# Performance work log

Measured on AMD Instinct MI355X. Metric: run time of the kernel, lower is better.

## Reference

```python
import jax, jax.numpy as jnp
import numpy as np

N = 100_000      # nodes
E = 500_000      # bonds
DN = 128         # dim_node_embedding
DB = 64          # dim_bond_embedding
NTOK = 4         # num_bond_token
DIN = 2 * DN + 2 * DB  # 384
LEAKY = 0.001
LN_EPS = 1e-5
DIST_MAX = 20.0
STEP = 0.5


def _lrelu(v):
    return jnp.where(v >= 0, v, LEAKY * v)


def _layernorm(v, w, b):
    m = v.mean(-1, keepdims=True)
    var = ((v - m) ** 2).mean(-1, keepdims=True)
    return (v - m) / jnp.sqrt(var + LN_EPS) * w + b


def setup_inputs() -> dict:
    key = jax.random.key(0)
    ks = jax.random.split(key, 20)
    x = jax.random.normal(ks[0], (N, 3), dtype=jnp.float32) * 3.0
    pos = jax.random.normal(ks[1], (N, 3), dtype=jnp.float32)
    node_embedding = jax.random.normal(ks[2], (N, DN), dtype=jnp.float32)
    i0 = jax.random.randint(ks[3], (E,), 0, N)
    off = jax.random.randint(ks[4], (E,), 1, N)  # nonzero -> no self-bonds
    bond_index = jnp.stack([i0, (i0 + off) % N], axis=1).astype(jnp.int32)
    bond_types = jax.random.randint(ks[5], (E,), 0, NTOK).astype(jnp.int32)
    s = 0.02
    params = dict(
        bond_emb=jax.random.normal(ks[6], (NTOK, DB), dtype=jnp.float32),
        W0=jax.random.normal(ks[7], (DIN, DN), dtype=jnp.float32) * s,
        b0=jnp.zeros((DN,), jnp.float32),
        W1=jax.random.normal(ks[8], (DN, DN), dtype=jnp.float32) * s,
        b1=jnp.zeros((DN,), jnp.float32),
        ln1_w=jnp.ones((DN,), jnp.float32),
        ln1_b=jnp.zeros((DN,), jnp.float32),
        W2=jax.random.normal(ks[9], (DN, DN), dtype=jnp.float32) * s,
        b2=jnp.zeros((DN,), jnp.float32),
        ln2_w=jnp.ones((DN,), jnp.float32),
        ln2_b=jnp.zeros((DN,), jnp.float32),
        Wo=jax.random.normal(ks[10], (DN, 2), dtype=jnp.float32) * s,
        bo=jnp.zeros((2,), jnp.float32),
    )
    return dict(x=x, pos=pos, node_embedding=node_embedding,
                bond_index=bond_index, bond_types=bond_types, **params)


def reference(x, pos, node_embedding, bond_index, bond_types,
              bond_emb, W0, b0, W1, b1, ln1_w, ln1_b,
              W2, b2, ln2_w, ln2_b, Wo, bo):
    i = bond_index[:, 0]
    j = bond_index[:, 1]

    # ---- BondLength geometry ----
    diff = x[i] - x[j]                                   # [E,3]
    dist = jnp.linalg.norm(diff, axis=-1, keepdims=True)  # [E,1]
    u = diff / dist                                       # [E,3] unit j->i? (i-j)/d
    direction = jnp.stack([u, -u], axis=-1)               # [E,3,2]

    # ---- Smearing (gaussian RBF + overflow bin, normalized) ----
    offset = jnp.linspace(0.0, DIST_MAX, DB - 1, dtype=jnp.float32)  # [63]
    delta = DIST_MAX / (DB - 2)
    coeff = -0.5 / (delta * delta)
    rbf = jnp.exp(coeff * (dist - offset) ** 2)            # [E,63]
    ovf = (dist >= DIST_MAX).astype(x.dtype)               # [E,1]
    smear = jnp.concatenate([rbf, ovf], axis=-1)           # [E,64]
    smear = smear / smear.sum(axis=-1, keepdims=True)

    # ---- Edge MLP (LeakyMLP, num_layer=2, dim_end=2) ----
    feat = jnp.concatenate(
        [node_embedding[i], node_embedding[j], bond_emb[bond_types], smear],
        axis=-1)                                           # [E,384]
    h = _lrelu(feat @ W0 + b0)
    h = _lrelu(_layernorm(h @ W1 + b1, ln1_w, ln1_b))
    h = _lrelu(_layernorm(h @ W2 + b2, ln2_w, ln2_b))
    force = h @ Wo + bo                                    # [E,2]

    # ---- position update (scatter-add) ----
    update = force[:, None, :] * direction                 # [E,3,2]
    pos = pos.at[i].add(STEP * update[..., 0])
    pos = pos.at[j].add(STEP * update[..., 1])
    return pos
```

## Files before the change

### kernel.cpp

```cpp
#include <hip/hip_runtime.h>
#include <stdint.h>

#define N_EDGES 500000
#define N_NODES 100000

typedef __attribute__((ext_vector_type(8))) short short8;
typedef __attribute__((ext_vector_type(4))) float floatx4;

__device__ __forceinline__ uint16_t f2bf(float f) {
  union { float f; uint32_t u; } cv; cv.f = f;
  uint32_t u = cv.u;
  return (uint16_t)((u + 0x7FFFu + ((u >> 16) & 1u)) >> 16);
}
__device__ __forceinline__ uint32_t pk2bf(float lo, float hi) {
  return __builtin_amdgcn_perm(__float_as_uint(hi), __float_as_uint(lo), 0x07060302u);
}
__device__ __forceinline__ uint16_t bftrunc(float f) {
  return (uint16_t)(__float_as_uint(f) >> 16);
}
__device__ __forceinline__ float bf2f_lo(uint32_t u) {
  return __uint_as_float(u << 16);
}
__device__ __forceinline__ float bf2f_hi(uint32_t u) {
  return __uint_as_float(u & 0xFFFF0000u);
}
__device__ __forceinline__ float lrelu(float v) { return fmaxf(v, 0.001f * v); }

__global__ void prep0_kernel(const float* __restrict__ W0, const float* __restrict__ b0,
                             const float* __restrict__ W1, const float* __restrict__ W2,
                             const float* __restrict__ bemb,
                             uint16_t* __restrict__ w0ab, uint16_t* __restrict__ w0c,
                             uint16_t* __restrict__ w1f, uint16_t* __restrict__ w2f,
                             float* __restrict__ be0f,
                             const float* __restrict__ pos, float* __restrict__ out, int npos) {
  int id = blockIdx.x * 256 + threadIdx.x;
  if (id < 32768) {
    int f = id;
    int j = f & 7, lane = (f >> 3) & 63, ntt = (f >> 9) & 15, ks = f >> 13;
    int k = ks * 32 + (lane >> 4) * 8 + j;
    int row = (ntt < 8) ? k : (128 + k);
    int col = (ntt & 7) * 16 + (lane & 15);
    w0ab[f] = f2bf(W0[row * 128 + col]);
  } else if (id < 40960) {
    int f = id - 32768;
    int j = f & 7, lane = (f >> 3) & 63, nt = (f >> 9) & 7, ks = f >> 12;
    int k = ks * 32 + (lane >> 4) * 8 + j;
    w0c[f] = f2bf(W0[(320 + k) * 128 + nt * 16 + (lane & 15)]);
  } else if (id < 57344) {
    int f = id - 40960;
    int j = f & 7, lane = (f >> 3) & 63, nt = (f >> 9) & 7, ks = f >> 12;
    int k = ks * 32 + (lane >> 4) * 8 + j;
    w1f[f] = f2bf(W1[k * 128 + nt * 16 + (lane & 15)]);
  } else if (id < 73728) {
    int f = id - 57344;
    int j = f & 7, lane = (f >> 3) & 63, nt = (f >> 9) & 7, ks = f >> 12;
    int k = ks * 32 + (lane >> 4) * 8 + j;
    w2f[f] = f2bf(W2[k * 128 + nt * 16 + (lane & 15)]);
  } else if (id < 74240) {
    int t = id - 73728; int ty = t >> 7, n = t & 127;
    float s = b0[n];
    for (int kk = 0; kk < 64; ++kk) s += bemb[ty * 64 + kk] * W0[(256 + kk) * 128 + n];
    be0f[t] = s;
  } else if (id - 74240 < npos) {
    out[id - 74240] = pos[id - 74240];
  }
}

__global__ __attribute__((amdgpu_flat_work_group_size(256, 256), amdgpu_waves_per_eu(3, 3)))
void prep_p_kernel(const float* __restrict__ nemb, const uint16_t* __restrict__ w0ab,
                   uint16_t* __restrict__ Pa, uint16_t* __restrict__ Pb) {
  __shared__ __align__(16) uint16_t aLds[4 * 16 * 136];
  const int tid = threadIdx.x;
  const int lane = tid & 63;
  const int wave = tid >> 6;
  const int n15 = lane & 15;
  const int quad = lane >> 4;
  uint16_t* myA = aLds + wave * (16 * 136);
  const int base = blockIdx.x * 64 + wave * 16;

  {
    const int le = lane >> 2, sub = lane & 3;
    int r = base + le; if (r >= N_NODES) r = N_NODES - 1;
    const float4* src = (const float4*)(nemb + (size_t)r * 128);
#pragma unroll
    for (int g = 0; g < 4; ++g) {
      float4 a = src[sub * 8 + g * 2], b = src[sub * 8 + g * 2 + 1];
      uint4 pk;
      pk.x = pk2bf(a.x, a.y); pk.y = pk2bf(a.z, a.w);
      pk.z = pk2bf(b.x, b.y); pk.w = pk2bf(b.z, b.w);
      *(uint4*)(myA + le * 136 + sub * 32 + g * 8) = pk;
    }
  }

  floatx4 acc[16];
#pragma unroll
  for (int t = 0; t < 16; ++t) acc[t] = (floatx4){0.f, 0.f, 0.f, 0.f};
  const short8* wfv = (const short8*)w0ab + lane;
#pragma unroll
  for (int ks = 0; ks < 4; ++ks) {
    short8 a = *(const short8*)(myA + n15 * 136 + ks * 32 + quad * 8);
    short8 b[16];
#pragma unroll
    for (int ntt = 0; ntt < 16; ++ntt) b[ntt] = wfv[(ks * 16 + ntt) * 64];
#pragma unroll
    for (int ntt = 0; ntt < 16; ++ntt)
      acc[ntt] = __builtin_amdgcn_mfma_f32_16x16x32_bf16(a, b[ntt], acc[ntt], 0, 0, 0);
  }

#pragma unroll
  for (int p = 0; p < 2; ++p) {
#pragma unroll
    for (int nt = 0; nt < 8; ++nt)
#pragma unroll
      for (int r = 0; r < 4; ++r)
        myA[(quad * 4 + r) * 136 + nt * 16 + n15] = bftrunc(acc[p * 8 + nt][r]);
    const int le = lane >> 2, sub = lane & 3;
    int row = base + le;
    if (row < N_NODES) {
      uint16_t* dst = (p == 0 ? Pa : Pb) + (size_t)row * 128;
#pragma unroll
      for (int g = 0; g < 4; ++g)
        *(uint4*)(dst + sub * 32 + g * 8) =
            *(const uint4*)(myA + le * 136 + sub * 32 + g * 8);
    }
  }
}

template <int NKS>
__device__ __forceinline__ void gemm_fw(const uint16_t* __restrict__ wf,
                                        const uint16_t* aRow, int lane, floatx4* acc) {
  const short8* wfv = (const short8*)wf + lane;
  short8 a[NKS];
#pragma unroll
  for (int ks = 0; ks < NKS; ++ks) a[ks] = *(const short8*)(aRow + ks * 32);
  short8 b0[8], b1[8];
#pragma unroll
  for (int nt = 0; nt < 8; ++nt) b0[nt] = wfv[nt * 64];
#pragma unroll
  for (int ks = 0; ks < NKS; ++ks) {
    const short8* cur = (ks & 1) ? b1 : b0;
    short8* nxt = (ks & 1) ? b0 : b1;
    if (ks + 1 < NKS) {
#pragma unroll
      for (int nt = 0; nt < 8; ++nt) nxt[nt] = wfv[((ks + 1) * 8 + nt) * 64];
    }
#pragma unroll
    for (int nt = 0; nt < 8; ++nt)
      acc[nt] = __builtin_amdgcn_mfma_f32_16x16x32_bf16(a[ks], cur[nt], acc[nt], 0, 0, 0);
  }
}

__global__ __attribute__((amdgpu_flat_work_group_size(256, 256), amdgpu_waves_per_eu(3, 3)))
void bond_mlp_kernel(const float* __restrict__ x,
                     const int* __restrict__ bidx, const int* __restrict__ btyp,
                     const uint16_t* __restrict__ Pa, const uint16_t* __restrict__ Pb,
                     const uint16_t* __restrict__ w0c, const uint16_t* __restrict__ w1f,
                     const uint16_t* __restrict__ w2f, const float* __restrict__ be0f,
                     const float* __restrict__ b1, const float* __restrict__ ln1w,
                     const float* __restrict__ ln1b,
                     const float* __restrict__ b2, const float* __restrict__ ln2w,
                     const float* __restrict__ ln2b,
                     const float* __restrict__ Wo, const float* __restrict__ bo,
                     float* __restrict__ out) {
  __shared__ __align__(16) uint16_t wlds[4 * 5312];
  __shared__ float u_lds[64][3];
  __shared__ int ij_lds[64][2];
  __shared__ int type_lds[64];

  const int tid = threadIdx.x;
  const int lane = tid & 63;
  const int wave = tid >> 6;
  const int n15 = lane & 15;
  const int quad = lane >> 4;

  uint16_t* base16 = wlds + wave * 5312;
  float* h0pre = (float*)base16;
  uint16_t* hA = base16;
  uint16_t* smearA = base16 + 4160;

  {
    const int le = lane >> 2, sub = lane & 3;
    const int lrow = le;
    const int ge = blockIdx.x * 64 + wave * 16 + le;
    const bool valid = ge < N_EDGES;
    int vi = 0, vj = 0, bt = 0;
    if (valid) { vi = bidx[2 * ge]; vj = bidx[2 * ge + 1]; bt = btyp[ge]; }
    float dx, dy, dz;
    if (valid) {
      dx = x[3 * vi]     - x[3 * vj];
      dy = x[3 * vi + 1] - x[3 * vj + 1];
      dz = x[3 * vi + 2] - x[3 * vj + 2];
    } else { dx = 1.0f; dy = 0.0f; dz = 0.0f; }
    float dist = sqrtf(dx * dx + dy * dy + dz * dz);
    float rinv = 1.0f / dist;
    if (sub == 0) {
      int gr = wave * 16 + lrow;
      u_lds[gr][0] = dx * rinv; u_lds[gr][1] = dy * rinv; u_lds[gr][2] = dz * rinv;
      ij_lds[gr][0] = vi; ij_lds[gr][1] = vj; type_lds[gr] = bt;
    }
    const uint4* pa = (const uint4*)(Pa + (size_t)vi * 128);
    const uint4* pb = (const uint4*)(Pb + (size_t)vj * 128);
    const float4* bbp = (const float4*)(be0f + bt * 128);
#pragma unroll
    for (int g = 0; g < 4; ++g) {
      uint4 av = pa[sub * 4 + g];
      uint4 bv = pb[sub * 4 + g];
      float4 e0 = bbp[sub * 8 + g * 2], e1 = bbp[sub * 8 + g * 2 + 1];
      float4 s0, s1;
      s0.x = bf2f_lo(av.x) + bf2f_lo(bv.x) + e0.x;
      s0.y = bf2f_hi(av.x) + bf2f_hi(bv.x) + e0.y;
      s0.z = bf2f_lo(av.y) + bf2f_lo(bv.y) + e0.z;
      s0.w = bf2f_hi(av.y) + bf2f_hi(bv.y) + e0.w;
      s1.x = bf2f_lo(av.z) + bf2f_lo(bv.z) + e1.x;
      s1.y = bf2f_hi(av.z) + bf2f_hi(bv.z) + e1.y;
      s1.z = bf2f_lo(av.w) + bf2f_lo(bv.w) + e1.z;
      s1.w = bf2f_hi(av.w) + bf2f_hi(bv.w) + e1.w;
      *(float4*)(h0pre + lrow * 130 + sub * 32 + g * 8) = s0;
      *(float4*)(h0pre + lrow * 130 + sub * 32 + g * 8 + 4) = s1;
    }
    const float delta = 20.0f / 62.0f;
    const float coeff = -0.5f / (delta * delta);
    float sv[16]; float ssum = 0.0f;
#pragma unroll
    for (int t = 0; t < 16; ++t) {
      int kk = sub * 16 + t;
      float v;
      if (kk < 63) { float d = dist - (float)kk * delta; v = __expf(coeff * d * d); }
      else v = (dist >= 20.0f) ? 1.0f : 0.0f;
      sv[t] = v; ssum += v;
    }
    ssum += __shfl_xor(ssum, 1);
    ssum += __shfl_xor(ssum, 2);
    float sinv = 1.0f / ssum;
#pragma unroll
    for (int g = 0; g < 2; ++g) {
      uint4 pk;
      pk.x = pk2bf(sv[g*8+0]*sinv, sv[g*8+1]*sinv);
      pk.y = pk2bf(sv[g*8+2]*sinv, sv[g*8+3]*sinv);
      pk.z = pk2bf(sv[g*8+4]*sinv, sv[g*8+5]*sinv);
      pk.w = pk2bf(sv[g*8+6]*sinv, sv[g*8+7]*sinv);
      *(uint4*)(smearA + lrow * 72 + sub * 16 + g * 8) = pk;
    }
  }

  floatx4 acc[8];
#pragma unroll
  for (int nt = 0; nt < 8; ++nt)
#pragma unroll
    for (int r = 0; r < 4; ++r)
      acc[nt][r] = h0pre[(quad * 4 + r) * 130 + nt * 16 + n15];

  gemm_fw<2>(w0c, smearA + n15 * 72 + quad * 8, lane, acc);

#pragma unroll
  for (int nt = 0; nt < 8; ++nt)
#pragma unroll
    for (int r = 0; r < 4; ++r)
      hA[(quad * 4 + r) * 136 + nt * 16 + n15] = bftrunc(lrelu(acc[nt][r]));

#pragma unroll
  for (int nt = 0; nt < 8; ++nt) acc[nt] = (floatx4){0.f, 0.f, 0.f, 0.f};
  gemm_fw<4>(w1f, hA + n15 * 136 + quad * 8, lane, acc);

  {
    float bv[8], wv[8], bb2[8];
#pragma unroll
    for (int nt = 0; nt < 8; ++nt) {
      int col = nt * 16 + n15;
      bv[nt] = b1[col]; wv[nt] = ln1w[col]; bb2[nt] = ln1b[col];
    }
    float s[4] = {0,0,0,0}, q[4] = {0,0,0,0};
#pragma unroll
    for (int nt = 0; nt < 8; ++nt)
#pragma unroll
      for (int r = 0; r < 4; ++r) { float v = acc[nt][r] + bv[nt]; s[r] += v; q[r] += v * v; }
#pragma unroll
    for (int m = 1; m <= 8; m <<= 1)
#pragma unroll
      for (int r = 0; r < 4; ++r) { s[r] += __shfl_xor(s[r], m); q[r] += __shfl_xor(q[r], m); }
    float mean[4], rstd[4];
#pragma unroll
    for (int r = 0; r < 4; ++r) {
      mean[r] = s[r] * (1.0f / 128.0f);
      float var = q[r] * (1.0f / 128.0f) - mean[r] * mean[r];
      rstd[r] = rsqrtf(var + 1e-5f);
    }
#pragma unroll
    for (int nt = 0; nt < 8; ++nt)
#pragma unroll
      for (int r = 0; r < 4; ++r) {
        float v = acc[nt][r] + bv[nt];
        float vn = (v - mean[r]) * rstd[r] * wv[nt] + bb2[nt];
        hA[(quad * 4 + r) * 136 + nt * 16 + n15] = bftrunc(lrelu(vn));
      }
  }

#pragma unroll
  for (int nt = 0; nt < 8; ++nt) acc[nt] = (floatx4){0.f, 0.f, 0.f, 0.f};
  gemm_fw<4>(w2f, hA + n15 * 136 + quad * 8, lane, acc);

  {
    float bv[8], wv[8], bb2[8], wo0[8], wo1[8];
#pragma unroll
    for (int nt = 0; nt < 8; ++nt) {
      int col = nt * 16 + n15;
      bv[nt] = b2[col]; wv[nt] = ln2w[col]; bb2[nt] = ln2b[col];
      wo0[nt] = Wo[2 * col]; wo1[nt] = Wo[2 * col + 1];
    }
    float s[4] = {0,0,0,0}, q[4] = {0,0,0,0};
#pragma unroll
    for (int nt = 0; nt < 8; ++nt)
#pragma unroll
      for (int r = 0; r < 4; ++r) { float v = acc[nt][r] + bv[nt]; s[r] += v; q[r] += v * v; }
#pragma unroll
    for (int m = 1; m <= 8; m <<= 1)
#pragma unroll
      for (int r = 0; r < 4; ++r) { s[r] += __shfl_xor(s[r], m); q[r] += __shfl_xor(q[r], m); }
    float mean[4], rstd[4];
#pragma unroll
    for (int r = 0; r < 4; ++r) {
      mean[r] = s[r] * (1.0f / 128.0f);
      float var = q[r] * (1.0f / 128.0f) - mean[r] * mean[r];
      rstd[r] = rsqrtf(var + 1e-5f);
    }
    float f0[4] = {0,0,0,0}, f1[4] = {0,0,0,0};
#pragma unroll
    for (int nt = 0; nt < 8; ++nt)
#pragma unroll
      for (int r = 0; r < 4; ++r) {
        float v = acc[nt][r] + bv[nt];
        float vn = lrelu((v - mean[r]) * rstd[r] * wv[nt] + bb2[nt]);
        f0[r] += vn * wo0[nt];
        f1[r] += vn * wo1[nt];
      }
#pragma unroll
    for (int m = 1; m <= 8; m <<= 1)
#pragma unroll
      for (int r = 0; r < 4; ++r) { f0[r] += __shfl_xor(f0[r], m); f1[r] += __shfl_xor(f1[r], m); }

    if (n15 < 4) {
      int gr = wave * 16 + quad * 4 + n15;
      int ge2 = blockIdx.x * 64 + gr;
      if (ge2 < N_EDGES) {
        float F0 = (n15 == 0) ? f0[0] : (n15 == 1) ? f0[1] : (n15 == 2) ? f0[2] : f0[3];
        float F1 = (n15 == 0) ? f1[0] : (n15 == 1) ? f1[1] : (n15 == 2) ? f1[2] : f1[3];
        F0 += bo[0]; F1 += bo[1];
        float ux = u_lds[gr][0], uy = u_lds[gr][1], uz = u_lds[gr][2];
        int ii = ij_lds[gr][0], jj = ij_lds[gr][1];
        float c0 = 0.5f * F0;
        float c1 = -0.5f * F1;
        atomicAdd(out + 3 * ii,     c0 * ux);
        atomicAdd(out + 3 * ii + 1, c0 * uy);
        atomicAdd(out + 3 * ii + 2, c0 * uz);
        atomicAdd(out + 3 * jj,     c1 * ux);
        atomicAdd(out + 3 * jj + 1, c1 * uy);
        atomicAdd(out + 3 * jj + 2, c1 * uz);
      }
    }
  }
}

extern "C" void kernel_launch(void* const* d_in, const int* in_sizes, int n_in,
                              void* d_out, int out_size, void* d_ws, size_t ws_size,
                              hipStream_t stream) {
  const float* x    = (const float*)d_in[0];
  const float* pos  = (const float*)d_in[1];
  const float* nemb = (const float*)d_in[2];
  const int*   bidx = (const int*)d_in[3];
  const int*   btyp = (const int*)d_in[4];
  const float* bemb = (const float*)d_in[5];
  const float* W0   = (const float*)d_in[6];
  const float* b0   = (const float*)d_in[7];
  const float* W1   = (const float*)d_in[8];
  const float* b1   = (const float*)d_in[9];
  const float* ln1w = (const float*)d_in[10];
  const float* ln1b = (const float*)d_in[11];
  const float* W2   = (const float*)d_in[12];
  const float* b2   = (const float*)d_in[13];
  const float* ln2w = (const float*)d_in[14];
  const float* ln2b = (const float*)d_in[15];
  const float* Wo   = (const float*)d_in[16];
  const float* bo   = (const float*)d_in[17];
  float* out = (float*)d_out;

  uint16_t* w0ab = (uint16_t*)d_ws;
  uint16_t* w0c  = w0ab + 32768;
  uint16_t* w1f  = w0c + 8192;
  uint16_t* w2f  = w1f + 16384;
  float*    be0f = (float*)(w2f + 16384);
  uint16_t* Pa   = (uint16_t*)(be0f + 512);
  uint16_t* Pb   = Pa + (size_t)N_NODES * 128;

  prep0_kernel<<<(74240 + out_size + 255) / 256, 256, 0, stream>>>(
      W0, b0, W1, W2, bemb, w0ab, w0c, w1f, w2f, be0f, pos, out, out_size);
  prep_p_kernel<<<(N_NODES + 63) / 64, 256, 0, stream>>>(nemb, w0ab, Pa, Pb);
  bond_mlp_kernel<<<(N_EDGES + 63) / 64, 256, 0, stream>>>(
      x, bidx, btyp, Pa, Pb, w0c, w1f, w2f, be0f,
      b1, ln1w, ln1b, b2, ln2w, ln2b, Wo, bo, out);
}
```

Measured before the change: 362.6 us.

## Shrink LDS in bond MLP, batch node rows in prep, drop weight double-buffer

The bond MLP kernel now stores the gathered first-layer partial sums as bf16 instead of fp32 in LDS, which shrinks its per-wave LDS footprint. Its waves_per_eu pin is removed and the weight double-buffer in gemm_fw is dropped to lower register pressure, both aimed at higher occupancy. The node-projection prep kernel processes two 16-row groups per wave, reuses each weight fragment across them, and writes results straight to global memory with scalar 16-bit stores instead of staging through LDS. The bf16 round-trip adds rounding error to the first-layer preactivation, and the scattered 2-byte stores may coalesce poorly.

Result: faster. 353.7 us (-2.4%).

```diff
diff --git a/kernel.cpp b/kernel.cpp
--- a/kernel.cpp
+++ b/kernel.cpp
@@ -3,6 +3,7 @@
 
 #define N_EDGES 500000
 #define N_NODES 100000
+#define PREP_NG 2
 
 typedef __attribute__((ext_vector_type(8))) short short8;
 typedef __attribute__((ext_vector_type(4))) float floatx4;
@@ -17,6 +18,9 @@
 }
 __device__ __forceinline__ uint16_t bftrunc(float f) {
   return (uint16_t)(__float_as_uint(f) >> 16);
+}
+__device__ __forceinline__ float bfup(uint16_t h) {
+  return __uint_as_float(((uint32_t)h) << 16);
 }
 __device__ __forceinline__ float bf2f_lo(uint32_t u) {
   return __uint_as_float(u << 16);
@@ -66,62 +70,67 @@
   }
 }
 
-__global__ __attribute__((amdgpu_flat_work_group_size(256, 256), amdgpu_waves_per_eu(3, 3)))
+__global__ __attribute__((amdgpu_flat_work_group_size(256, 256), amdgpu_waves_per_eu(1, 4)))
 void prep_p_kernel(const float* __restrict__ nemb, const uint16_t* __restrict__ w0ab,
                    uint16_t* __restrict__ Pa, uint16_t* __restrict__ Pb) {
-  __shared__ __align__(16) uint16_t aLds[4 * 16 * 136];
+  __shared__ __align__(16) uint16_t aLds[4 * PREP_NG * 16 * 136];
   const int tid = threadIdx.x;
   const int lane = tid & 63;
   const int wave = tid >> 6;
   const int n15 = lane & 15;
   const int quad = lane >> 4;
-  uint16_t* myA = aLds + wave * (16 * 136);
-  const int base = blockIdx.x * 64 + wave * 16;
+  uint16_t* myA = aLds + wave * (PREP_NG * 16 * 136);
+  const int base = blockIdx.x * (64 * PREP_NG) + wave * (16 * PREP_NG);
 
   {
     const int le = lane >> 2, sub = lane & 3;
-    int r = base + le; if (r >= N_NODES) r = N_NODES - 1;
-    const float4* src = (const float4*)(nemb + (size_t)r * 128);
-#pragma unroll
-    for (int g = 0; g < 4; ++g) {
-      float4 a = src[sub * 8 + g * 2], b = src[sub * 8 + g * 2 + 1];
-      uint4 pk;
-      pk.x = pk2bf(a.x, a.y); pk.y = pk2bf(a.z, a.w);
-      pk.z = pk2bf(b.x, b.y); pk.w = pk2bf(b.z, b.w);
-      *(uint4*)(myA + le * 136 + sub * 32 + g * 8) = pk;
-    }
-  }
-
-  floatx4 acc[16];
-#pragma unroll
-  for (int t = 0; t < 16; ++t) acc[t] = (floatx4){0.f, 0.f, 0.f, 0.f};
+#pragma unroll
+    for (int it = 0; it < PREP_NG; ++it) {
+      int r = base + it * 16 + le; if (r >= N_NODES) r = N_NODES - 1;
+      const float4* src = (const float4*)(nemb + (size_t)r * 128);
+#pragma unroll
+      for (int g = 0; g < 4; ++g) {
+        float4 a = src[sub * 8 + g * 2], b = src[sub * 8 + g * 2 + 1];
+        uint4 pk;
+        pk.x = pk2bf(a.x, a.y); pk.y = pk2bf(a.z, a.w);
+        pk.z = pk2bf(b.x, b.y); pk.w = pk2bf(b.z, b.w);
+        *(uint4*)(myA + (it * 16 + le) * 136 + sub * 32 + g * 8) = pk;
+      }
+    }
+  }
+
   const short8* wfv = (const short8*)w0ab + lane;
 #pragma unroll
-  for (int ks = 0; ks < 4; ++ks) {
-    short8 a = *(const short8*)(myA + n15 * 136 + ks * 32 + quad * 8);
-    short8 b[16];
-#pragma unroll
-    for (int ntt = 0; ntt < 16; ++ntt) b[ntt] = wfv[(ks * 16 + ntt) * 64];
-#pragma unroll
-    for (int ntt = 0; ntt < 16; ++ntt)
-      acc[ntt] = __builtin_amdgcn_mfma_f32_16x16x32_bf16(a, b[ntt], acc[ntt], 0, 0, 0);
-  }
-
-#pragma unroll
-  for (int p = 0; p < 2; ++p) {
-#pragma unroll
-    for (int nt = 0; nt < 8; ++nt)
-#pragma unroll
-      for (int r = 0; r < 4; ++r)
-        myA[(quad * 4 + r) * 136 + nt * 16 + n15] = bftrunc(acc[p * 8 + nt][r]);
-    const int le = lane >> 2, sub = lane & 3;
-    int row = base + le;
-    if (row < N_NODES) {
-      uint16_t* dst = (p == 0 ? Pa : Pb) + (size_t)row * 128;
-#pragma unroll
-      for (int g = 0; g < 4; ++g)
-        *(uint4*)(dst + sub * 32 + g * 8) =
-            *(const uint4*)(myA + le * 136 + sub * 32 + g * 8);
+  for (int q = 0; q < 4; ++q) {
+    short8 bfr[16];
+#pragma unroll
+    for (int ks = 0; ks < 4; ++ks)
+#pragma unroll
+      for (int nq = 0; nq < 4; ++nq)
+        bfr[ks * 4 + nq] = wfv[(ks * 16 + q * 4 + nq) * 64];
+#pragma unroll
+    for (int it = 0; it < PREP_NG; ++it) {
+      floatx4 acc[4];
+#pragma unroll
+      for (int nq = 0; nq < 4; ++nq) acc[nq] = (floatx4){0.f, 0.f, 0.f, 0.f};
+#pragma unroll
+      for (int ks = 0; ks < 4; ++ks) {
+        short8 a = *(const short8*)(myA + (it * 16 + n15) * 136 + ks * 32 + quad * 8);
+#pragma unroll
+        for (int nq = 0; nq < 4; ++nq)
+          acc[nq] = __builtin_amdgcn_mfma_f32_16x16x32_bf16(a, bfr[ks * 4 + nq], acc[nq], 0, 0, 0);
+      }
+      uint16_t* dst = (q < 2) ? Pa : Pb;
+      int cbase = ((q & 1) * 4) * 16 + n15;
+#pragma unroll
+      for (int nq = 0; nq < 4; ++nq) {
+        int c = cbase + nq * 16;
+#pragma unroll
+        for (int r = 0; r < 4; ++r) {
+          int row = base + it * 16 + quad * 4 + r;
+          if (row < N_NODES) dst[(size_t)row * 128 + c] = bftrunc(acc[nq][r]);
+        }
+      }
     }
   }
 }
@@ -133,24 +142,17 @@
   short8 a[NKS];
 #pragma unroll
   for (int ks = 0; ks < NKS; ++ks) a[ks] = *(const short8*)(aRow + ks * 32);
-  short8 b0[8], b1[8];
-#pragma unroll
-  for (int nt = 0; nt < 8; ++nt) b0[nt] = wfv[nt * 64];
 #pragma unroll
   for (int ks = 0; ks < NKS; ++ks) {
-    const short8* cur = (ks & 1) ? b1 : b0;
-    short8* nxt = (ks & 1) ? b0 : b1;
-    if (ks + 1 < NKS) {
-#pragma unroll
-      for (int nt = 0; nt < 8; ++nt) nxt[nt] = wfv[((ks + 1) * 8 + nt) * 64];
-    }
-#pragma unroll
-    for (int nt = 0; nt < 8; ++nt)
-      acc[nt] = __builtin_amdgcn_mfma_f32_16x16x32_bf16(a[ks], cur[nt], acc[nt], 0, 0, 0);
-  }
-}
-
-__global__ __attribute__((amdgpu_flat_work_group_size(256, 256), amdgpu_waves_per_eu(3, 3)))
+#pragma unroll
+    for (int nt = 0; nt < 8; ++nt) {
+      short8 b = wfv[(ks * 8 + nt) * 64];
+      acc[nt] = __builtin_amdgcn_mfma_f32_16x16x32_bf16(a[ks], b, acc[nt], 0, 0, 0);
+    }
+  }
+}
+
+__global__ __attribute__((amdgpu_flat_work_group_size(256, 256)))
 void bond_mlp_kernel(const float* __restrict__ x,
                      const int* __restrict__ bidx, const int* __restrict__ btyp,
                      const uint16_t* __restrict__ Pa, const uint16_t* __restrict__ Pb,
@@ -162,7 +164,7 @@
                      const float* __restrict__ ln2b,
                      const float* __restrict__ Wo, const float* __restrict__ bo,
                      float* __restrict__ out) {
-  __shared__ __align__(16) uint16_t wlds[4 * 5312];
+  __shared__ __align__(16) uint16_t wlds[4 * 3328];
   __shared__ float u_lds[64][3];
   __shared__ int ij_lds[64][2];
   __shared__ int type_lds[64];
@@ -173,10 +175,8 @@
   const int n15 = lane & 15;
   const int quad = lane >> 4;
 
-  uint16_t* base16 = wlds + wave * 5312;
-  float* h0pre = (float*)base16;
-  uint16_t* hA = base16;
-  uint16_t* smearA = base16 + 4160;
+  uint16_t* hA = wlds + wave * 3328;
+  uint16_t* smearA = hA + 2176;
 
   {
     const int le = lane >> 2, sub = lane & 3;
@@ -206,17 +206,16 @@
       uint4 av = pa[sub * 4 + g];
       uint4 bv = pb[sub * 4 + g];
       float4 e0 = bbp[sub * 8 + g * 2], e1 = bbp[sub * 8 + g * 2 + 1];
-      float4 s0, s1;
-      s0.x = bf2f_lo(av.x) + bf2f_lo(bv.x) + e0.x;
-      s0.y = bf2f_hi(av.x) + bf2f_hi(bv.x) + e0.y;
-      s0.z = bf2f_lo(av.y) + bf2f_lo(bv.y) + e0.z;
-      s0.w = bf2f_hi(av.y) + bf2f_hi(bv.y) + e0.w;
-      s1.x = bf2f_lo(av.z) + bf2f_lo(bv.z) + e1.x;
-      s1.y = bf2f_hi(av.z) + bf2f_hi(bv.z) + e1.y;
-      s1.z = bf2f_lo(av.w) + bf2f_lo(bv.w) + e1.z;
-      s1.w = bf2f_hi(av.w) + bf2f_hi(bv.w) + e1.w;
-      *(float4*)(h0pre + lrow * 130 + sub * 32 + g * 8) = s0;
-      *(float4*)(h0pre + lrow * 130 + sub * 32 + g * 8 + 4) = s1;
+      uint4 pk;
+      pk.x = pk2bf(bf2f_lo(av.x) + bf2f_lo(bv.x) + e0.x,
+                   bf2f_hi(av.x) + bf2f_hi(bv.x) + e0.y);
+      pk.y = pk2bf(bf2f_lo(av.y) + bf2f_lo(bv.y) + e0.z,
+                   bf2f_hi(av.y) + bf2f_hi(bv.y) + e0.w);
+      pk.z = pk2bf(bf2f_lo(av.z) + bf2f_lo(bv.z) + e1.x,
+                   bf2f_hi(av.z) + bf2f_hi(bv.z) + e1.y);
+      pk.w = pk2bf(bf2f_lo(av.w) + bf2f_lo(bv.w) + e1.z,
+                   bf2f_hi(av.w) + bf2f_hi(bv.w) + e1.w);
+      *(uint4*)(hA + lrow * 136 + sub * 32 + g * 8) = pk;
     }
     const float delta = 20.0f / 62.0f;
     const float coeff = -0.5f / (delta * delta);
@@ -248,7 +247,7 @@
   for (int nt = 0; nt < 8; ++nt)
 #pragma unroll
     for (int r = 0; r < 4; ++r)
-      acc[nt][r] = h0pre[(quad * 4 + r) * 130 + nt * 16 + n15];
+      acc[nt][r] = bfup(hA[(quad * 4 + r) * 136 + nt * 16 + n15]);
 
   gemm_fw<2>(w0c, smearA + n15 * 72 + quad * 8, lane, acc);
 
@@ -393,7 +392,8 @@
 
   prep0_kernel<<<(74240 + out_size + 255) / 256, 256, 0, stream>>>(
       W0, b0, W1, W2, bemb, w0ab, w0c, w1f, w2f, be0f, pos, out, out_size);
-  prep_p_kernel<<<(N_NODES + 63) / 64, 256, 0, stream>>>(nemb, w0ab, Pa, Pb);
+  prep_p_kernel<<<(N_NODES + 64 * PREP_NG - 1) / (64 * PREP_NG), 256, 0, stream>>>(
+      nemb, w0ab, Pa, Pb);
   bond_mlp_kernel<<<(N_EDGES + 63) / 64, 256, 0, stream>>>(
       x, bidx, btyp, Pa, Pb, w0c, w1f, w2f, be0f,
       b1, ln1w, ln1b, b2, ln2w, ln2b, Wo, bo, out);
```
